# Kernel optimization log

Hardware: AMD Instinct MI355X
Metric: run time of the kernel (lower is better)

## Reference

```python
import jax, jax.numpy as jnp
import numpy as np

HID = 128

def _gru_states(x, w_ih, w_hh, b_ih, b_hh):
    # x: [B,T,I]; w_ih: [3H,I]; w_hh: [3H,H]; biases: [3H]
    # Precompute input projections for all timesteps (one big GEMM).
    gi = jnp.einsum('bti,gi->tbg', x, w_ih) + b_ih  # [T,B,3H]
    B = x.shape[0]
    h0 = jnp.zeros((B, HID), dtype=x.dtype)

    def step(h, gi_t):
        gh = h @ w_hh.T + b_hh                      # [B,3H]
        i_r, i_z, i_n = jnp.split(gi_t, 3, axis=-1)
        h_r, h_z, h_n = jnp.split(gh, 3, axis=-1)
        r = jax.nn.sigmoid(i_r + h_r)
        z = jax.nn.sigmoid(i_z + h_z)
        n = jnp.tanh(i_n + r * h_n)
        h_new = (1.0 - z) * n + z * h
        return h_new, h_new

    _, states = jax.lax.scan(step, h0, gi)          # states: [T,B,H]
    return states


def setup_inputs() -> dict:
    key = jax.random.key(0)
    ks = jax.random.split(key, 7)
    B, T, I, H, E = 64, 2048, 128, HID, 64
    s_ih = 1.0 / np.sqrt(I)
    s_hh = 1.0 / np.sqrt(H)
    s_p = 1.0 / np.sqrt(H)
    return {
        'x': jax.random.normal(ks[0], (B, T, I), dtype=jnp.float32),
        'w_ih': jax.random.uniform(ks[1], (3 * H, I), jnp.float32, -s_ih, s_ih),
        'w_hh': jax.random.uniform(ks[2], (3 * H, H), jnp.float32, -s_hh, s_hh),
        'b_ih': jax.random.uniform(ks[3], (3 * H,), jnp.float32, -s_hh, s_hh),
        'b_hh': jax.random.uniform(ks[4], (3 * H,), jnp.float32, -s_hh, s_hh),
        'w_proj': jax.random.uniform(ks[5], (E, H), jnp.float32, -s_p, s_p),
        'b_proj': jax.random.uniform(ks[6], (E,), jnp.float32, -s_p, s_p),
    }


def reference(x, w_ih, w_hh, b_ih, b_hh, w_proj, b_proj):
    states = _gru_states(x, w_ih, w_hh, b_ih, b_hh)  # [T,B,H]
    pooled = states.mean(axis=0)                     # mean pooling over time -> [B,H]
    return pooled @ w_proj.T + b_proj                # [B,E]
```

## Files before the change

### kernel.cpp

```cpp
#include <hip/hip_runtime.h>
#include <math.h>

#define B_   64
#define T_   2048
#define HID_ 128
#define G3_  384
#define IN_  128
#define E_   64

#define TS_  128

typedef _Float16 h2f  __attribute__((ext_vector_type(2)));
typedef _Float16 f16x8 __attribute__((ext_vector_type(8)));
typedef float    f32x4 __attribute__((ext_vector_type(4)));

#define L2E  1.4426950408889634f
#define L2E2 2.8853900817779268f

#if __has_builtin(__builtin_amdgcn_exp2f)
#define EXP2(x) __builtin_amdgcn_exp2f(x)
#else
#define EXP2(x) __expf((x) * 0.6931471805599453f)
#endif

__device__ __forceinline__ float rcp_(float x)     { return __builtin_amdgcn_rcpf(x); }
__device__ __forceinline__ float sigmoid_(float x) { return rcp_(1.f + __expf(-x)); }
__device__ __forceinline__ float tanh_(float x)    { return 1.f - 2.f * rcp_(1.f + __expf(2.f * x)); }

__device__ __forceinline__ f16x8 pack8_(float4 a, float4 b) {
    uint4 u;
    u.x = __builtin_bit_cast(unsigned, __builtin_amdgcn_cvt_pkrtz(a.x, a.y));
    u.y = __builtin_bit_cast(unsigned, __builtin_amdgcn_cvt_pkrtz(a.z, a.w));
    u.z = __builtin_bit_cast(unsigned, __builtin_amdgcn_cvt_pkrtz(b.x, b.y));
    u.w = __builtin_bit_cast(unsigned, __builtin_amdgcn_cvt_pkrtz(b.z, b.w));
    return __builtin_bit_cast(f16x8, u);
}

__global__ __launch_bounds__(256, 1)
void gi_gemm(const float* __restrict__ x, const float* __restrict__ w_ih,
             const float* __restrict__ b_ih, const float* __restrict__ b_hh,
             float* __restrict__ gi, int t0)
{
    const int tid = threadIdx.x;
    const int w   = tid >> 6;
    const int l   = tid & 63;
    const int ln  = l & 15;
    const int kq  = l >> 4;
    const int tt  = blockIdx.x;
    const int b   = blockIdx.y;
    const int tl_base = tt * TS_ + w * 32;

    float bias_r[24];
    #pragma unroll
    for (int nt = 0; nt < 24; nt++) {
        const int col = nt * 16 + ln;
        bias_r[nt] = b_ih[col] + (col < 256 ? b_hh[col] : 0.f);
    }

    f32x4 acc[2][24];
    #pragma unroll
    for (int mt = 0; mt < 2; mt++)
        #pragma unroll
        for (int nt = 0; nt < 24; nt++)
            acc[mt][nt] = (f32x4){0.f, 0.f, 0.f, 0.f};

    const float* xb = x + ((size_t)b * T_ + (size_t)(t0 + tl_base)) * IN_;

    #pragma unroll
    for (int kc = 0; kc < 4; kc++) {
        const int ko = kc * 32 + kq * 8;
        f16x8 afr[2];
        #pragma unroll
        for (int mt = 0; mt < 2; mt++) {
            const float* xr = xb + (size_t)(mt * 16 + ln) * IN_ + ko;
            float4 p0 = *reinterpret_cast<const float4*>(xr);
            float4 p1 = *reinterpret_cast<const float4*>(xr + 4);
            afr[mt] = pack8_(p0, p1);
        }
        #pragma unroll
        for (int nt = 0; nt < 24; nt++) {
            const float* wr = w_ih + (size_t)(nt * 16 + ln) * IN_ + ko;
            float4 q0 = *reinterpret_cast<const float4*>(wr);
            float4 q1 = *reinterpret_cast<const float4*>(wr + 4);
            const f16x8 bfr = pack8_(q0, q1);
            acc[0][nt] = __builtin_amdgcn_mfma_f32_16x16x32_f16(afr[0], bfr, acc[0][nt], 0, 0, 0);
            acc[1][nt] = __builtin_amdgcn_mfma_f32_16x16x32_f16(afr[1], bfr, acc[1][nt], 0, 0, 0);
        }
    }

    #pragma unroll
    for (int mt = 0; mt < 2; mt++) {
        #pragma unroll
        for (int r = 0; r < 4; r++) {
            const size_t trow = (size_t)(tl_base + mt * 16 + kq * 4 + r);
            float* go = gi + trow * (B_ * G3_) + (size_t)b * G3_ + ln;
            #pragma unroll
            for (int nt = 0; nt < 24; nt++)
                go[nt * 16] = acc[mt][nt][r] + bias_r[nt];
        }
    }
}

#define REC_STEP(CUR, LD, TLOAD, PB)                                           \
  {                                                                            \
    const float* gp_ = gib + (size_t)(TLOAD) * S;                              \
    LD[0] = gp_[cg]; LD[1] = gp_[cg + 128]; LD[2] = gp_[cg + 256];             \
    const char* hb_ = (const char*)(&h2_sh[PB][0]) + kq * 16;                  \
    f16x8 af_[4];                                                              \
    af_[0] = __builtin_bit_cast(f16x8, *(const uint4*)(hb_));                  \
    af_[1] = __builtin_bit_cast(f16x8, *(const uint4*)(hb_ + 64));             \
    af_[2] = __builtin_bit_cast(f16x8, *(const uint4*)(hb_ + 128));            \
    af_[3] = __builtin_bit_cast(f16x8, *(const uint4*)(hb_ + 192));            \
    f32x4 ac_[3];                                                              \
    _Pragma("unroll")                                                          \
    for (int g = 0; g < 3; g++) ac_[g] = (f32x4){0.f, 0.f, 0.f, 0.f};          \
    _Pragma("unroll")                                                          \
    for (int kc = 0; kc < 4; kc++) {                                           \
      _Pragma("unroll")                                                        \
      for (int g = 0; g < 3; g++)                                              \
        ac_[g] = __builtin_amdgcn_mfma_f32_16x16x32_f16(af_[kc], wf[g][kc],    \
                                                        ac_[g], 0, 0, 0);      \
    }                                                                          \
    const float q_  = CUR[2] * L2E2;                                           \
    const float yr_ = fmaf(CUR[0], L2E, ac_[0][0]);                            \
    const float r_  = rcp_(1.f + EXP2(-yr_));                                  \
    const float yz_ = fmaf(CUR[1], L2E, ac_[1][0]);                            \
    const float z_  = rcp_(1.f + EXP2(-yz_));                                  \
    const float yn_ = fmaf(r_, ac_[2][0] + bh, q_);                            \
    const float u_  = rcp_(1.f + EXP2(yn_));                                   \
    const float n_  = fmaf(-2.f, u_, 1.f);                                     \
    hj = n_ + z_ * (hj - n_);                                                  \
    hs += hj;                                                                  \
    if (kq == 0) h2_sh[(PB) ^ 1][cg] = (_Float16)hj;                           \
    __syncthreads();                                                           \
  }

__global__ __launch_bounds__(512, 2)
void rec_kernel(const float* __restrict__ gi, const float* __restrict__ w_hh,
                const float* __restrict__ b_hh,
                const float* __restrict__ w_proj, const float* __restrict__ b_proj,
                float* __restrict__ out, float* __restrict__ state,
                int t0, int t1)
{
    const int tid  = threadIdx.x;
    const int b    = blockIdx.x;
    const int w    = tid >> 6;
    const int lane = tid & 63;
    const int ln   = lane & 15;
    const int kq   = lane >> 4;
    const int wh   = w & 3;
    const int f    = w >> 2;
    const int cg   = 16 * wh + ln + 64 * f;
    const int nT   = t1 - t0;

    __shared__ _Float16 h2_sh[2][HID_];
    __shared__ float pooled[HID_];

    f16x8 wf[3][4];
    #pragma unroll
    for (int g = 0; g < 3; g++) {
        const float s = (g == 2) ? L2E2 : L2E;
        const float* wr = w_hh + (size_t)(128 * g + cg) * HID_;
        #pragma unroll
        for (int kc = 0; kc < 4; kc++) {
            const float* p = wr + kc * 32 + kq * 8;
            float4 q0 = *reinterpret_cast<const float4*>(p);
            float4 q1 = *reinterpret_cast<const float4*>(p + 4);
            q0.x *= s; q0.y *= s; q0.z *= s; q0.w *= s;
            q1.x *= s; q1.y *= s; q1.z *= s; q1.w *= s;
            wf[g][kc] = pack8_(q0, q1);
        }
    }
    const float bh = L2E2 * b_hh[256 + cg];

    float hj, hs;
    if (t0 == 0) { hj = hs = 0.f; }
    else {
        hj = state[b * HID_ + cg];
        hs = state[B_ * HID_ + b * HID_ + cg];
    }
    if (kq == 0) h2_sh[0][cg] = (_Float16)hj;
    __syncthreads();

    const float* gib = gi + (size_t)b * G3_;
    const size_t S = (size_t)B_ * G3_;

    float g0[3], g1[3], g2[3], g3[3];
    {
        const float* p0 = gib;
        const float* p1 = gib + S;
        g0[0] = p0[cg]; g0[1] = p0[cg + 128]; g0[2] = p0[cg + 256];
        g1[0] = p1[cg]; g1[1] = p1[cg + 128]; g1[2] = p1[cg + 256];
    }

    int pb = 0;
    for (int t = 0; t < nT; t += 4) {
        const int nTm1 = nT - 1;
        int t2 = t + 2 < nTm1 ? t + 2 : nTm1;
        int t3 = t + 3 < nTm1 ? t + 3 : nTm1;
        int t4 = t + 4 < nTm1 ? t + 4 : nTm1;
        int t5 = t + 5 < nTm1 ? t + 5 : nTm1;
        REC_STEP(g0, g2, t2, pb); pb ^= 1;
        REC_STEP(g1, g3, t3, pb); pb ^= 1;
        REC_STEP(g2, g0, t4, pb); pb ^= 1;
        REC_STEP(g3, g1, t5, pb); pb ^= 1;
    }

    if (t1 < T_) {
        if (kq == 0) {
            state[b * HID_ + cg]             = hj;
            state[B_ * HID_ + b * HID_ + cg] = hs;
        }
    } else {
        if (kq == 0) pooled[cg] = hs * (1.f / (float)T_);
        __syncthreads();
        if (tid < E_) {
            const float4* wpj = reinterpret_cast<const float4*>(w_proj + (size_t)tid * HID_);
            const float4* pp  = reinterpret_cast<const float4*>(pooled);
            float a0 = 0.f, a1 = 0.f, a2 = 0.f, a3 = 0.f;
            #pragma unroll
            for (int k = 0; k < 32; k++) {
                float4 wv = wpj[k]; float4 pv = pp[k];
                a0 = fmaf(wv.x, pv.x, a0);
                a1 = fmaf(wv.y, pv.y, a1);
                a2 = fmaf(wv.z, pv.z, a2);
                a3 = fmaf(wv.w, pv.w, a3);
            }
            out[b * E_ + tid] = (a0 + a1) + (a2 + a3) + b_proj[tid];
        }
    }
}

extern "C" void kernel_launch(void* const* d_in, const int* in_sizes, int n_in,
                              void* d_out, int out_size, void* d_ws, size_t ws_size,
                              hipStream_t stream)
{
    const float* x      = (const float*)d_in[0];
    const float* w_ih   = (const float*)d_in[1];
    const float* w_hh   = (const float*)d_in[2];
    const float* b_ih   = (const float*)d_in[3];
    const float* b_hh   = (const float*)d_in[4];
    const float* w_proj = (const float*)d_in[5];
    const float* b_proj = (const float*)d_in[6];
    float* out = (float*)d_out;

    const size_t state_bytes = (size_t)2 * B_ * HID_ * sizeof(float);
    const size_t per_t = (size_t)B_ * G3_ * sizeof(float);
    size_t avail = ws_size > state_bytes ? ws_size - state_bytes : 0;
    int chunkT = (int)(avail / per_t);
    if (chunkT > T_) chunkT = T_;
    chunkT &= ~(TS_ - 1);
    if (chunkT < TS_) chunkT = TS_;

    float* gi_buf = (float*)d_ws;
    float* state  = (float*)((char*)d_ws + (size_t)chunkT * per_t);

    for (int t0 = 0; t0 < T_; t0 += chunkT) {
        int t1 = t0 + chunkT; if (t1 > T_) t1 = T_;
        int nT = t1 - t0;
        gi_gemm<<<dim3(nT / TS_, B_), dim3(256), 0, stream>>>(x, w_ih, b_ih, b_hh, gi_buf, t0);
        rec_kernel<<<dim3(B_), dim3(512), 0, stream>>>(gi_buf, w_hh, b_hh, w_proj, b_proj,
                                                       out, state, t0, t1);
    }
}
```

Before: 848.5 us.

## Overlap input-projection GEMM with recurrence via double-buffered fused chunk launches

Merges the GEMM and recurrence kernels into one launch in which the first blocks run the recurrence for chunk i-1 and the remaining blocks compute the input projections for chunk i into the other half of a double buffer. The GEMM now runs 512 threads with 16 rows per wave and two 12-tile halves to cut register pressure. Chunks of 256 timesteps give nine launches, so GEMM work can fill CUs left idle by the 64 recurrence blocks. The cost is more launches, and GEMM blocks share the device with the latency-bound recurrence blocks, which may slow them.

```diff
diff --git a/kernel.cpp b/kernel.cpp
--- a/kernel.cpp
+++ b/kernel.cpp
@@ -9,8 +9,8 @@
 #define E_   64
 
 #define TS_  128
-
-typedef _Float16 h2f  __attribute__((ext_vector_type(2)));
+#define CT_  256
+
 typedef _Float16 f16x8 __attribute__((ext_vector_type(8)));
 typedef float    f32x4 __attribute__((ext_vector_type(4)));
 
@@ -23,9 +23,7 @@
 #define EXP2(x) __expf((x) * 0.6931471805599453f)
 #endif
 
-__device__ __forceinline__ float rcp_(float x)     { return __builtin_amdgcn_rcpf(x); }
-__device__ __forceinline__ float sigmoid_(float x) { return rcp_(1.f + __expf(-x)); }
-__device__ __forceinline__ float tanh_(float x)    { return 1.f - 2.f * rcp_(1.f + __expf(2.f * x)); }
+__device__ __forceinline__ float rcp_(float x) { return __builtin_amdgcn_rcpf(x); }
 
 __device__ __forceinline__ f16x8 pack8_(float4 a, float4 b) {
     uint4 u;
@@ -36,81 +34,74 @@
     return __builtin_bit_cast(f16x8, u);
 }
 
-__global__ __launch_bounds__(256, 1)
-void gi_gemm(const float* __restrict__ x, const float* __restrict__ w_ih,
-             const float* __restrict__ b_ih, const float* __restrict__ b_hh,
-             float* __restrict__ gi, int t0)
+__device__ __forceinline__ void gemm_body(
+    int g, int nTiles, int t0,
+    const float* __restrict__ x, const float* __restrict__ w_ih,
+    const float* __restrict__ b_ih, const float* __restrict__ b_hh,
+    float* __restrict__ gi)
 {
     const int tid = threadIdx.x;
     const int w   = tid >> 6;
     const int l   = tid & 63;
     const int ln  = l & 15;
     const int kq  = l >> 4;
-    const int tt  = blockIdx.x;
-    const int b   = blockIdx.y;
-    const int tl_base = tt * TS_ + w * 32;
-
-    float bias_r[24];
-    #pragma unroll
-    for (int nt = 0; nt < 24; nt++) {
-        const int col = nt * 16 + ln;
-        bias_r[nt] = b_ih[col] + (col < 256 ? b_hh[col] : 0.f);
-    }
-
-    f32x4 acc[2][24];
-    #pragma unroll
-    for (int mt = 0; mt < 2; mt++)
-        #pragma unroll
-        for (int nt = 0; nt < 24; nt++)
-            acc[mt][nt] = (f32x4){0.f, 0.f, 0.f, 0.f};
+    const int tt  = g % nTiles;
+    const int b   = g / nTiles;
+    const int tl_base = tt * TS_ + w * 16;
 
     const float* xb = x + ((size_t)b * T_ + (size_t)(t0 + tl_base)) * IN_;
 
+    f16x8 afr[4];
     #pragma unroll
     for (int kc = 0; kc < 4; kc++) {
-        const int ko = kc * 32 + kq * 8;
-        f16x8 afr[2];
-        #pragma unroll
-        for (int mt = 0; mt < 2; mt++) {
-            const float* xr = xb + (size_t)(mt * 16 + ln) * IN_ + ko;
-            float4 p0 = *reinterpret_cast<const float4*>(xr);
-            float4 p1 = *reinterpret_cast<const float4*>(xr + 4);
-            afr[mt] = pack8_(p0, p1);
-        }
-        #pragma unroll
-        for (int nt = 0; nt < 24; nt++) {
-            const float* wr = w_ih + (size_t)(nt * 16 + ln) * IN_ + ko;
-            float4 q0 = *reinterpret_cast<const float4*>(wr);
-            float4 q1 = *reinterpret_cast<const float4*>(wr + 4);
-            const f16x8 bfr = pack8_(q0, q1);
-            acc[0][nt] = __builtin_amdgcn_mfma_f32_16x16x32_f16(afr[0], bfr, acc[0][nt], 0, 0, 0);
-            acc[1][nt] = __builtin_amdgcn_mfma_f32_16x16x32_f16(afr[1], bfr, acc[1][nt], 0, 0, 0);
-        }
+        const float* xr = xb + (size_t)ln * IN_ + kc * 32 + kq * 8;
+        float4 p0 = *reinterpret_cast<const float4*>(xr);
+        float4 p1 = *reinterpret_cast<const float4*>(xr + 4);
+        afr[kc] = pack8_(p0, p1);
     }
 
     #pragma unroll
-    for (int mt = 0; mt < 2; mt++) {
-        #pragma unroll
-        for (int r = 0; r < 4; r++) {
-            const size_t trow = (size_t)(tl_base + mt * 16 + kq * 4 + r);
-            float* go = gi + trow * (B_ * G3_) + (size_t)b * G3_ + ln;
+    for (int half = 0; half < 2; half++) {
+        f32x4 acc[12];
+        #pragma unroll
+        for (int j = 0; j < 12; j++) acc[j] = (f32x4){0.f, 0.f, 0.f, 0.f};
+
+        #pragma unroll
+        for (int kc = 0; kc < 4; kc++) {
             #pragma unroll
-            for (int nt = 0; nt < 24; nt++)
-                go[nt * 16] = acc[mt][nt][r] + bias_r[nt];
+            for (int j = 0; j < 12; j++) {
+                const int nt = half * 12 + j;
+                const float* wr = w_ih + (size_t)(nt * 16 + ln) * IN_ + kc * 32 + kq * 8;
+                float4 q0 = *reinterpret_cast<const float4*>(wr);
+                float4 q1 = *reinterpret_cast<const float4*>(wr + 4);
+                const f16x8 bfr = pack8_(q0, q1);
+                acc[j] = __builtin_amdgcn_mfma_f32_16x16x32_f16(afr[kc], bfr, acc[j], 0, 0, 0);
+            }
+        }
+
+        #pragma unroll
+        for (int j = 0; j < 12; j++) {
+            const int col = half * 192 + j * 16 + ln;
+            const float bias = b_ih[col] + (col < 256 ? b_hh[col] : 0.f);
+            #pragma unroll
+            for (int r = 0; r < 4; r++) {
+                const size_t trow = (size_t)(tl_base + kq * 4 + r);
+                gi[trow * (B_ * G3_) + (size_t)b * G3_ + col] = acc[j][r] + bias;
+            }
         }
     }
 }
 
 #define REC_STEP(CUR, LD, TLOAD, PB)                                           \
   {                                                                            \
-    const float* gp_ = gib + (size_t)(TLOAD) * S;                              \
-    LD[0] = gp_[cg]; LD[1] = gp_[cg + 128]; LD[2] = gp_[cg + 256];             \
     const char* hb_ = (const char*)(&h2_sh[PB][0]) + kq * 16;                  \
     f16x8 af_[4];                                                              \
     af_[0] = __builtin_bit_cast(f16x8, *(const uint4*)(hb_));                  \
     af_[1] = __builtin_bit_cast(f16x8, *(const uint4*)(hb_ + 64));             \
     af_[2] = __builtin_bit_cast(f16x8, *(const uint4*)(hb_ + 128));            \
     af_[3] = __builtin_bit_cast(f16x8, *(const uint4*)(hb_ + 192));            \
+    const float* gp_ = gib + (size_t)(TLOAD) * S;                              \
+    LD[0] = gp_[cg]; LD[1] = gp_[cg + 128]; LD[2] = gp_[cg + 256];             \
     f32x4 ac_[3];                                                              \
     _Pragma("unroll")                                                          \
     for (int g = 0; g < 3; g++) ac_[g] = (f32x4){0.f, 0.f, 0.f, 0.f};          \
@@ -135,15 +126,15 @@
     __syncthreads();                                                           \
   }
 
-__global__ __launch_bounds__(512, 2)
-void rec_kernel(const float* __restrict__ gi, const float* __restrict__ w_hh,
-                const float* __restrict__ b_hh,
-                const float* __restrict__ w_proj, const float* __restrict__ b_proj,
-                float* __restrict__ out, float* __restrict__ state,
-                int t0, int t1)
+__device__ __forceinline__ void rec_body(
+    int b,
+    const float* __restrict__ gi, const float* __restrict__ w_hh,
+    const float* __restrict__ b_hh,
+    const float* __restrict__ w_proj, const float* __restrict__ b_proj,
+    float* __restrict__ out, float* __restrict__ state,
+    int t0, int t1)
 {
     const int tid  = threadIdx.x;
-    const int b    = blockIdx.x;
     const int w    = tid >> 6;
     const int lane = tid & 63;
     const int ln   = lane & 15;
@@ -194,8 +185,8 @@
     }
 
     int pb = 0;
+    const int nTm1 = nT - 1;
     for (int t = 0; t < nT; t += 4) {
-        const int nTm1 = nT - 1;
         int t2 = t + 2 < nTm1 ? t + 2 : nTm1;
         int t3 = t + 3 < nTm1 ? t + 3 : nTm1;
         int t4 = t + 4 < nTm1 ? t + 4 : nTm1;
@@ -231,6 +222,23 @@
     }
 }
 
+__global__ __launch_bounds__(512, 1)
+void fused(const float* __restrict__ x, const float* __restrict__ w_ih,
+           const float* __restrict__ b_ih, const float* __restrict__ w_hh,
+           const float* __restrict__ b_hh,
+           const float* __restrict__ w_proj, const float* __restrict__ b_proj,
+           const float* __restrict__ gi_rec, float* __restrict__ gi_out,
+           float* __restrict__ out, float* __restrict__ state,
+           int trec0, int trec1, int tg0, int nRec, int nTiles)
+{
+    const int bid = (int)blockIdx.x;
+    if (bid < nRec) {
+        rec_body(bid, gi_rec, w_hh, b_hh, w_proj, b_proj, out, state, trec0, trec1);
+    } else {
+        gemm_body(bid - nRec, nTiles, tg0, x, w_ih, b_ih, b_hh, gi_out);
+    }
+}
+
 extern "C" void kernel_launch(void* const* d_in, const int* in_sizes, int n_in,
                               void* d_out, int out_size, void* d_ws, size_t ws_size,
                               hipStream_t stream)
@@ -246,20 +254,39 @@
 
     const size_t state_bytes = (size_t)2 * B_ * HID_ * sizeof(float);
     const size_t per_t = (size_t)B_ * G3_ * sizeof(float);
-    size_t avail = ws_size > state_bytes ? ws_size - state_bytes : 0;
-    int chunkT = (int)(avail / per_t);
-    if (chunkT > T_) chunkT = T_;
-    chunkT &= ~(TS_ - 1);
-    if (chunkT < TS_) chunkT = TS_;
-
-    float* gi_buf = (float*)d_ws;
-    float* state  = (float*)((char*)d_ws + (size_t)chunkT * per_t);
-
-    for (int t0 = 0; t0 < T_; t0 += chunkT) {
-        int t1 = t0 + chunkT; if (t1 > T_) t1 = T_;
-        int nT = t1 - t0;
-        gi_gemm<<<dim3(nT / TS_, B_), dim3(256), 0, stream>>>(x, w_ih, b_ih, b_hh, gi_buf, t0);
-        rec_kernel<<<dim3(B_), dim3(512), 0, stream>>>(gi_buf, w_hh, b_hh, w_proj, b_proj,
-                                                       out, state, t0, t1);
-    }
-}
+
+    if (ws_size >= 2 * (size_t)CT_ * per_t + state_bytes) {
+        float* buf[2] = { (float*)d_ws,
+                          (float*)((char*)d_ws + (size_t)CT_ * per_t) };
+        float* state  = (float*)((char*)d_ws + 2 * (size_t)CT_ * per_t);
+        const int nTiles = CT_ / TS_;
+        const int nC = T_ / CT_;
+        for (int i = 0; i <= nC; i++) {
+            const int rb = (i > 0)  ? B_ : 0;
+            const int gb = (i < nC) ? nTiles * B_ : 0;
+            fused<<<dim3(rb + gb), dim3(512), 0, stream>>>(
+                x, w_ih, b_ih, w_hh, b_hh, w_proj, b_proj,
+                buf[(i + 1) & 1] , buf[i & 1],
+                out, state,
+                (i - 1) * CT_, i * CT_, i * CT_, rb, nTiles);
+        }
+    } else {
+        size_t avail = ws_size > state_bytes ? ws_size - state_bytes : 0;
+        int cT = (int)(avail / per_t);
+        if (cT > T_) cT = T_;
+        cT &= ~(TS_ - 1);
+        if (cT < TS_) cT = TS_;
+        float* buf0  = (float*)d_ws;
+        float* state = (float*)((char*)d_ws + (size_t)cT * per_t);
+        for (int t0 = 0; t0 < T_; t0 += cT) {
+            int t1 = t0 + cT; if (t1 > T_) t1 = T_;
+            int nt = t1 - t0;
+            fused<<<dim3((nt / TS_) * B_), dim3(512), 0, stream>>>(
+                x, w_ih, b_ih, w_hh, b_hh, w_proj, b_proj,
+                buf0, buf0, out, state, 0, 0, t0, 0, nt / TS_);
+            fused<<<dim3(B_), dim3(512), 0, stream>>>(
+                x, w_ih, b_ih, w_hh, b_hh, w_proj, b_proj,
+                buf0, buf0, out, state, t0, t1, 0, B_, nt / TS_);
+        }
+    }
+}
```

After: 861.1 us. Within noise of the previous version (+1.5%).
